# Performance work log

Measured on AMD Instinct MI355X. Metric: run time of the kernel, lower is better.

The kernel has to match this reference:

```python
import jax, jax.numpy as jnp
import numpy as np

B, N, U = 4096, 128, 128  # batch, num_notes, num_units
F = N - 1                 # per-note feature dim; +1 condition scalar -> LSTM input = N
W_SCALE = 0.08            # ~1/sqrt(U), keeps gates in a sane range


def setup_inputs() -> dict:
    key = jax.random.key(0)
    ks = jax.random.split(key, 12)
    return {
        "note_features": jax.random.normal(ks[0], (B, N, F), jnp.float32),
        "targets": jax.random.uniform(ks[1], (B, N), jnp.float32),
        "w_ih0": jax.random.normal(ks[2], (4 * U, N), jnp.float32) * W_SCALE,
        "w_hh0": jax.random.normal(ks[3], (4 * U, U), jnp.float32) * W_SCALE,
        "b_ih0": jax.random.normal(ks[4], (4 * U,), jnp.float32) * W_SCALE,
        "b_hh0": jax.random.normal(ks[5], (4 * U,), jnp.float32) * W_SCALE,
        "w_ih1": jax.random.normal(ks[6], (4 * U, U), jnp.float32) * W_SCALE,
        "w_hh1": jax.random.normal(ks[7], (4 * U, U), jnp.float32) * W_SCALE,
        "b_ih1": jax.random.normal(ks[8], (4 * U,), jnp.float32) * W_SCALE,
        "b_hh1": jax.random.normal(ks[9], (4 * U,), jnp.float32) * W_SCALE,
        "w_out": jax.random.normal(ks[10], (1, U), jnp.float32) * W_SCALE,
        "b_out": jax.random.normal(ks[11], (1,), jnp.float32) * W_SCALE,
    }


def _lstm_cell(x, h, c, w_ih, w_hh, b_ih, b_hh):
    # PyTorch gate order: i, f, g, o
    gates = x @ w_ih.T + b_ih + h @ w_hh.T + b_hh  # [B, 4U]
    i, f, g, o = jnp.split(gates, 4, axis=-1)
    c_new = jax.nn.sigmoid(f) * c + jax.nn.sigmoid(i) * jnp.tanh(g)
    h_new = jax.nn.sigmoid(o) * jnp.tanh(c_new)
    return h_new, c_new


def reference(note_features, targets, w_ih0, w_hh0, b_ih0, b_hh0,
              w_ih1, w_hh1, b_ih1, b_hh1, w_out, b_out):
    b = note_features.shape[0]
    # teacher-forced condition: previous target note, zero at step 0
    cond = jnp.concatenate([jnp.zeros((b, 1), note_features.dtype), targets[:, :-1]], axis=1)
    x_seq = jnp.concatenate([note_features, cond[..., None]], axis=-1)  # [B, N, N]
    x_seq = jnp.transpose(x_seq, (1, 0, 2))                              # [N, B, N]

    zeros = jnp.zeros((b, U), note_features.dtype)

    def step(carry, x):
        h0, c0, h1, c1 = carry
        h0, c0 = _lstm_cell(x, h0, c0, w_ih0, w_hh0, b_ih0, b_hh0)
        h1, c1 = _lstm_cell(h0, h1, c1, w_ih1, w_hh1, b_ih1, b_hh1)
        return (h0, c0, h1, c1), h1

    _, hs = jax.lax.scan(step, (zeros, zeros, zeros, zeros), x_seq)  # [N, B, U]
    logits = jnp.einsum('nbu,ou->nbo', hs, w_out) + b_out            # [N, B, 1]
    return jnp.transpose(jax.nn.sigmoid(logits)[..., 0], (1, 0))     # [B, N]
```

## Files before the change

### kernel.cpp

```cpp
#include <hip/hip_runtime.h>
#include <math.h>

typedef _Float16 f16;
typedef _Float16 f16x8 __attribute__((ext_vector_type(8)));
typedef float f32x4 __attribute__((ext_vector_type(4)));

#define NSTEP 128
#define FEAT  127
#define BLK_B 16
#define NBLOCK 256
#define NTHREADS 512

__device__ __forceinline__ float sigf(float x) { return 1.0f / (1.0f + __expf(-x)); }
__device__ __forceinline__ float tanh_(float x) { return 1.0f - 2.0f / (1.0f + __expf(2.0f * x)); }

__device__ __forceinline__ void sync_lds() {
    asm volatile("s_waitcnt lgkmcnt(0)" ::: "memory");
    __builtin_amdgcn_s_barrier();
    asm volatile("" ::: "memory");
}

#define PIN(v) asm volatile("" : "+v"(v))

__device__ __forceinline__ f16x8 load_wfrag(const float* __restrict__ W, int n, int k) {
    const float* p = W + n * 128 + k;
    f16x8 r;
#pragma unroll
    for (int j = 0; j < 8; ++j) r[j] = (f16)p[j];
    return r;
}

__device__ __forceinline__ float row16_sum(float v) {
    int t;
    t = __builtin_amdgcn_update_dpp(0, __float_as_int(v), 0x118, 0xf, 0xf, true);
    v += __int_as_float(t);
    t = __builtin_amdgcn_update_dpp(0, __float_as_int(v), 0x114, 0xf, 0xf, true);
    v += __int_as_float(t);
    t = __builtin_amdgcn_update_dpp(0, __float_as_int(v), 0x112, 0xf, 0xf, true);
    v += __int_as_float(t);
    t = __builtin_amdgcn_update_dpp(0, __float_as_int(v), 0x111, 0xf, 0xf, true);
    v += __int_as_float(t);
    return v;
}

__global__ __launch_bounds__(NTHREADS, 2) void lstm_fused(
    const float* __restrict__ nf,    const float* __restrict__ tgt,
    const float* __restrict__ w_ih0, const float* __restrict__ w_hh0,
    const float* __restrict__ b_ih0, const float* __restrict__ b_hh0,
    const float* __restrict__ w_ih1, const float* __restrict__ w_hh1,
    const float* __restrict__ b_ih1, const float* __restrict__ b_hh1,
    const float* __restrict__ w_out, const float* __restrict__ b_out,
    f16* __restrict__ h0g, float* __restrict__ out)
{
    __shared__ __align__(16) f16 bufA[2][16][152];
    __shared__ __align__(16) f16 bufB[2][16][152];
    __shared__ float outp[2][8][16];

    const int tid  = threadIdx.x;
    const int wave = tid >> 6;
    const int lane = tid & 63;
    const int col  = lane & 15;
    const int quad = lane >> 4;
    const int b0   = blockIdx.x * BLK_B;
    const int u    = wave * 16 + col;
    const f32x4 zz = {0.f, 0.f, 0.f, 0.f};

    {
        for (int i = tid; i < 2 * 16 * 152; i += NTHREADS)
            (&bufB[0][0][0])[i] = (f16)0.0f;

        f32x4 bv0[4];
#pragma unroll
        for (int g = 0; g < 4; ++g) {
            const float b = b_ih0[g * 128 + u] + b_hh0[g * 128 + u];
            bv0[g] = (f32x4){b, b, b, b};
        }

        f16x8 wih0[4][4], whh0[4][4];
#pragma unroll
        for (int g = 0; g < 4; ++g)
#pragma unroll
            for (int ks = 0; ks < 4; ++ks) {
                wih0[g][ks] = load_wfrag(w_ih0, g * 128 + u, ks * 32 + quad * 8);
                whh0[g][ks] = load_wfrag(w_hh0, g * 128 + u, ks * 32 + quad * 8);
                PIN(wih0[g][ks]);
                PIN(whh0[g][ks]);
            }

        const float* px[2][2];
        int pxs[2][2];
#pragma unroll
        for (int rr = 0; rr < 2; ++rr) {
            const long rowg = b0 + wave * 2 + rr;
#pragma unroll
            for (int h = 0; h < 2; ++h) {
                const int k = lane + 64 * h;
                if (k < FEAT) { px[rr][h] = nf + (rowg * NSTEP + 2) * FEAT + k; pxs[rr][h] = FEAT; }
                else          { px[rr][h] = tgt + rowg * NSTEP + 1;             pxs[rr][h] = 1; }
            }
        }

        f16* hp = h0g + (long)(b0 + quad * 4) * NSTEP * 128 + u;

        f32x4 c0 = {0.f, 0.f, 0.f, 0.f};

#pragma unroll
        for (int rr = 0; rr < 2; ++rr) {
            const int row = wave * 2 + rr;
            const long gbt = (long)(b0 + row) * NSTEP;
#pragma unroll
            for (int h = 0; h < 2; ++h) {
                const int k = lane + 64 * h;
                bufA[0][row][k] = (f16)((k < FEAT) ? nf[gbt * FEAT + k] : 0.0f);
            }
        }

        float xb0[2][2], xb1[2][2];
#pragma unroll
        for (int rr = 0; rr < 2; ++rr) {
            const long rowg = b0 + wave * 2 + rr;
#pragma unroll
            for (int h = 0; h < 2; ++h) {
                const int k = lane + 64 * h;
                xb1[rr][h] = (k < FEAT) ? nf[(rowg * NSTEP + 1) * FEAT + k]
                                        : tgt[rowg * NSTEP];
            }
        }
        sync_lds();

        auto step0 = [&](int t, int pa, float (&xIssue)[2][2], float (&xWrite)[2][2]) {
            const int wb = pa ^ 1;

            if (t + 2 < NSTEP) {
#pragma unroll
                for (int rr = 0; rr < 2; ++rr)
#pragma unroll
                    for (int h = 0; h < 2; ++h) {
                        xIssue[rr][h] = *px[rr][h];
                        px[rr][h] += pxs[rr][h];
                    }
            }

            f16x8 ax[4], ah[4];
#pragma unroll
            for (int ks = 0; ks < 4; ++ks) {
                ax[ks] = *(const f16x8*)&bufA[pa][col][ks * 32 + quad * 8];
                ah[ks] = *(const f16x8*)&bufB[pa][col][ks * 32 + quad * 8];
            }

            f32x4 accx[4], acch[4];
#pragma unroll
            for (int g = 0; g < 4; ++g) {
                accx[g] = __builtin_amdgcn_mfma_f32_16x16x32_f16(ax[0], wih0[g][0], bv0[g], 0, 0, 0);
                acch[g] = __builtin_amdgcn_mfma_f32_16x16x32_f16(ah[0], whh0[g][0], zz, 0, 0, 0);
            }
#pragma unroll
            for (int ks = 1; ks < 4; ++ks)
#pragma unroll
                for (int g = 0; g < 4; ++g) {
                    accx[g] = __builtin_amdgcn_mfma_f32_16x16x32_f16(ax[ks], wih0[g][ks], accx[g], 0, 0, 0);
                    acch[g] = __builtin_amdgcn_mfma_f32_16x16x32_f16(ah[ks], whh0[g][ks], acch[g], 0, 0, 0);
                }

            float h0n[4];
#pragma unroll
            for (int r = 0; r < 4; ++r) {
                const float ig = sigf(accx[0][r] + acch[0][r]);
                const float fg = sigf(accx[1][r] + acch[1][r]);
                const float gg = tanh_(accx[2][r] + acch[2][r]);
                const float og = sigf(accx[3][r] + acch[3][r]);
                const float cn = fg * c0[r] + ig * gg;
                c0[r] = cn;
                h0n[r] = og * tanh_(cn);
            }
#pragma unroll
            for (int r = 0; r < 4; ++r) {
                bufB[wb][quad * 4 + r][u] = (f16)h0n[r];
                hp[r * (NSTEP * 128)] = (f16)h0n[r];
            }
            hp += 128;

            if (t + 1 < NSTEP) {
#pragma unroll
                for (int rr = 0; rr < 2; ++rr)
#pragma unroll
                    for (int h = 0; h < 2; ++h)
                        bufA[wb][wave * 2 + rr][lane + 64 * h] = (f16)xWrite[rr][h];
            }
            sync_lds();
        };

        for (int t2 = 0; t2 < NSTEP; t2 += 2) {
            step0(t2,     0, xb0, xb1);
            step0(t2 + 1, 1, xb1, xb0);
        }
    }

    __syncthreads();
    for (int i = tid; i < 2 * 16 * 152; i += NTHREADS)
        (&bufA[0][0][0])[i] = (f16)0.0f;
    __syncthreads();

    {
        f32x4 bv1[4];
#pragma unroll
        for (int g = 0; g < 4; ++g) {
            const float b = b_ih1[g * 128 + u] + b_hh1[g * 128 + u];
            bv1[g] = (f32x4){b, b, b, b};
        }
        const float wo_u = w_out[u];
        const float bout = b_out[0];

        f16x8 wih1[4][4], whh1[4][4];
#pragma unroll
        for (int g = 0; g < 4; ++g)
#pragma unroll
            for (int ks = 0; ks < 4; ++ks) {
                wih1[g][ks] = load_wfrag(w_ih1, g * 128 + u, ks * 32 + quad * 8);
                whh1[g][ks] = load_wfrag(w_hh1, g * 128 + u, ks * 32 + quad * 8);
                PIN(wih1[g][ks]);
                PIN(whh1[g][ks]);
            }

        f32x4 c1 = {0.f, 0.f, 0.f, 0.f};

        const f16* hrow = h0g + (long)(b0 + col) * NSTEP * 128 + quad * 8;
        f16x8 nxA[4], nxB[4];
#pragma unroll
        for (int ks = 0; ks < 4; ++ks)
            nxA[ks] = *(const f16x8*)(hrow + ks * 32);
#pragma unroll
        for (int ks = 0; ks < 4; ++ks)
            nxB[ks] = *(const f16x8*)(hrow + 128 + ks * 32);
        const f16* hnext = hrow + 256;

        auto step1 = [&](int t, int pa, f16x8 (&nxUse)[4]) {
            const int wb = pa ^ 1;

            f16x8 ahv[4];
#pragma unroll
            for (int ks = 0; ks < 4; ++ks)
                ahv[ks] = *(const f16x8*)&bufA[pa][col][ks * 32 + quad * 8];

            f32x4 accx[4], acch[4];
#pragma unroll
            for (int g = 0; g < 4; ++g) {
                accx[g] = __builtin_amdgcn_mfma_f32_16x16x32_f16(nxUse[0], wih1[g][0], bv1[g], 0, 0, 0);
                acch[g] = __builtin_amdgcn_mfma_f32_16x16x32_f16(ahv[0], whh1[g][0], zz, 0, 0, 0);
            }
#pragma unroll
            for (int ks = 1; ks < 4; ++ks)
#pragma unroll
                for (int g = 0; g < 4; ++g) {
                    accx[g] = __builtin_amdgcn_mfma_f32_16x16x32_f16(nxUse[ks], wih1[g][ks], accx[g], 0, 0, 0);
                    acch[g] = __builtin_amdgcn_mfma_f32_16x16x32_f16(ahv[ks], whh1[g][ks], acch[g], 0, 0, 0);
                }

            if (t + 2 < NSTEP) {
#pragma unroll
                for (int ks = 0; ks < 4; ++ks)
                    nxUse[ks] = *(const f16x8*)(hnext + ks * 32);
                hnext += 128;
            }

            float h1n[4];
#pragma unroll
            for (int r = 0; r < 4; ++r) {
                const float ig = sigf(accx[0][r] + acch[0][r]);
                const float fg = sigf(accx[1][r] + acch[1][r]);
                const float gg = tanh_(accx[2][r] + acch[2][r]);
                const float og = sigf(accx[3][r] + acch[3][r]);
                const float cn = fg * c1[r] + ig * gg;
                c1[r] = cn;
                h1n[r] = og * tanh_(cn);
            }
#pragma unroll
            for (int r = 0; r < 4; ++r)
                bufA[wb][quad * 4 + r][u] = (f16)h1n[r];

            float ps[4];
#pragma unroll
            for (int r = 0; r < 4; ++r) ps[r] = row16_sum(h1n[r] * wo_u);
            if (col == 15) {
#pragma unroll
                for (int r = 0; r < 4; ++r) outp[pa][wave][quad * 4 + r] = ps[r];
            }

            sync_lds();

            if (tid < 16) {
                float s = bout;
#pragma unroll
                for (int w = 0; w < 8; ++w) s += outp[pa][w][tid];
                out[(long)(b0 + tid) * NSTEP + t] = sigf(s);
            }
        };

        for (int t2 = 0; t2 < NSTEP; t2 += 2) {
            step1(t2,     0, nxA);
            step1(t2 + 1, 1, nxB);
        }
    }
}

__global__ void prep_weights(const float* __restrict__ w_ih0,
                             const float* __restrict__ w_hh0,
                             const float* __restrict__ w_ih1,
                             const float* __restrict__ w_hh1,
                             f16* __restrict__ ws16)
{
    int idx = blockIdx.x * blockDim.x + threadIdx.x;
    int j    = idx & 7;
    int lane = (idx >> 3) & 63;
    int ks   = (idx >> 9) & 3;
    int gate = (idx >> 11) & 3;
    int wave = (idx >> 13) & 7;
    int sel  = (idx >> 16) & 3;
    int n = gate * 128 + wave * 16 + (lane & 15);
    int k = ks * 32 + (lane >> 4) * 8 + j;
    const float* W = (sel == 0) ? w_ih0 : (sel == 1) ? w_hh0 : (sel == 2) ? w_ih1 : w_hh1;
    ws16[idx] = (f16)W[n * 128 + k];
}

__global__ __launch_bounds__(NTHREADS, 2) void lstm_fb(
    const float* __restrict__ nf,   const float* __restrict__ tgt,
    const float* __restrict__ b_ih0, const float* __restrict__ b_hh0,
    const float* __restrict__ b_ih1, const float* __restrict__ b_hh1,
    const float* __restrict__ w_out, const float* __restrict__ b_out,
    const f16* __restrict__ wfrag,  float* __restrict__ out)
{
    __shared__ f16 xs[2][16][152];
    __shared__ f16 h0s[2][16][152];
    __shared__ f16 h1s[2][16][152];
    __shared__ float outp[8][16];

    const int tid  = threadIdx.x;
    const int wave = tid >> 6;
    const int lane = tid & 63;
    const int col  = lane & 15;
    const int quad = lane >> 4;
    const int b0   = blockIdx.x * BLK_B;
    const int u    = wave * 16 + col;

    for (int i = tid; i < 2 * 16 * 152; i += NTHREADS) {
        (&h0s[0][0][0])[i] = (f16)0.0f;
        (&h1s[0][0][0])[i] = (f16)0.0f;
    }
    float bias0[4], bias1[4];
#pragma unroll
    for (int g = 0; g < 4; ++g) {
        bias0[g] = b_ih0[g * 128 + u] + b_hh0[g * 128 + u];
        bias1[g] = b_ih1[g * 128 + u] + b_hh1[g * 128 + u];
    }
    const float wo_u = w_out[u];
    const float bout = b_out[0];
    const f16x8* wf = (const f16x8*)wfrag;

    f32x4 c0 = {0.f, 0.f, 0.f, 0.f};
    f32x4 c1 = {0.f, 0.f, 0.f, 0.f};

#pragma unroll
    for (int rr = 0; rr < 2; ++rr) {
        const int row = wave * 2 + rr;
        const long gbt = (long)(b0 + row) * NSTEP;
#pragma unroll
        for (int h = 0; h < 2; ++h) {
            const int k = lane + 64 * h;
            xs[0][row][k] = (f16)((k < FEAT) ? nf[gbt * FEAT + k] : 0.0f);
        }
    }
    __syncthreads();

    for (int t = 0; t < NSTEP; ++t) {
        const int pa = t & 1, wb = pa ^ 1;
        float xnv[2][2];
#pragma unroll
        for (int rr = 0; rr < 2; ++rr) {
            const int row = wave * 2 + rr;
#pragma unroll
            for (int h = 0; h < 2; ++h) {
                const int k = lane + 64 * h;
                float v = 0.0f;
                if (t + 1 < NSTEP) {
                    const long gbt = (long)(b0 + row) * NSTEP + (t + 1);
                    v = (k < FEAT) ? nf[gbt * FEAT + k] : tgt[(long)(b0 + row) * NSTEP + t];
                }
                xnv[rr][h] = v;
            }
        }
        f32x4 acc[4];
#pragma unroll
        for (int g = 0; g < 4; ++g) acc[g] = (f32x4){bias0[g], bias0[g], bias0[g], bias0[g]};
#pragma unroll
        for (int ks = 0; ks < 4; ++ks) {
            f16x8 a = *(const f16x8*)&xs[pa][col][ks * 32 + quad * 8];
#pragma unroll
            for (int g = 0; g < 4; ++g) {
                f16x8 b = wf[((wave * 4 + g) * 4 + ks) * 64 + lane];
                acc[g] = __builtin_amdgcn_mfma_f32_16x16x32_f16(a, b, acc[g], 0, 0, 0);
            }
        }
#pragma unroll
        for (int ks = 0; ks < 4; ++ks) {
            f16x8 a = *(const f16x8*)&h0s[pa][col][ks * 32 + quad * 8];
#pragma unroll
            for (int g = 0; g < 4; ++g) {
                f16x8 b = wf[1 * 8192 + ((wave * 4 + g) * 4 + ks) * 64 + lane];
                acc[g] = __builtin_amdgcn_mfma_f32_16x16x32_f16(a, b, acc[g], 0, 0, 0);
            }
        }
        float h0n[4];
#pragma unroll
        for (int r = 0; r < 4; ++r) {
            const float ig = sigf(acc[0][r]);
            const float fg = sigf(acc[1][r]);
            const float gg = tanh_(acc[2][r]);
            const float og = sigf(acc[3][r]);
            const float cn = fg * c0[r] + ig * gg;
            c0[r] = cn;
            h0n[r] = og * tanh_(cn);
        }
#pragma unroll
        for (int r = 0; r < 4; ++r) h0s[wb][quad * 4 + r][u] = (f16)h0n[r];
        __syncthreads();

#pragma unroll
        for (int g = 0; g < 4; ++g) acc[g] = (f32x4){bias1[g], bias1[g], bias1[g], bias1[g]};
#pragma unroll
        for (int ks = 0; ks < 4; ++ks) {
            f16x8 a = *(const f16x8*)&h0s[wb][col][ks * 32 + quad * 8];
#pragma unroll
            for (int g = 0; g < 4; ++g) {
                f16x8 b = wf[2 * 8192 + ((wave * 4 + g) * 4 + ks) * 64 + lane];
                acc[g] = __builtin_amdgcn_mfma_f32_16x16x32_f16(a, b, acc[g], 0, 0, 0);
            }
        }
#pragma unroll
        for (int ks = 0; ks < 4; ++ks) {
            f16x8 a = *(const f16x8*)&h1s[pa][col][ks * 32 + quad * 8];
#pragma unroll
            for (int g = 0; g < 4; ++g) {
                f16x8 b = wf[3 * 8192 + ((wave * 4 + g) * 4 + ks) * 64 + lane];
                acc[g] = __builtin_amdgcn_mfma_f32_16x16x32_f16(a, b, acc[g], 0, 0, 0);
            }
        }
        float h1n[4];
#pragma unroll
        for (int r = 0; r < 4; ++r) {
            const float ig = sigf(acc[0][r]);
            const float fg = sigf(acc[1][r]);
            const float gg = tanh_(acc[2][r]);
            const float og = sigf(acc[3][r]);
            const float cn = fg * c1[r] + ig * gg;
            c1[r] = cn;
            h1n[r] = og * tanh_(cn);
        }
#pragma unroll
        for (int r = 0; r < 4; ++r) h1s[wb][quad * 4 + r][u] = (f16)h1n[r];
#pragma unroll
        for (int rr = 0; rr < 2; ++rr) {
            const int row = wave * 2 + rr;
#pragma unroll
            for (int h = 0; h < 2; ++h) xs[wb][row][lane + 64 * h] = (f16)xnv[rr][h];
        }
        float ps[4];
#pragma unroll
        for (int r = 0; r < 4; ++r) ps[r] = h1n[r] * wo_u;
#pragma unroll
        for (int m = 1; m < 16; m <<= 1) {
#pragma unroll
            for (int r = 0; r < 4; ++r) ps[r] += __shfl_xor(ps[r], m, 64);
        }
        if (col == 0) {
#pragma unroll
            for (int r = 0; r < 4; ++r) outp[wave][quad * 4 + r] = ps[r];
        }
        __syncthreads();
        if (tid < 16) {
            float s = bout;
#pragma unroll
            for (int w = 0; w < 8; ++w) s += outp[w][tid];
            out[(long)(b0 + tid) * NSTEP + t] = sigf(s);
        }
    }
}

extern "C" void kernel_launch(void* const* d_in, const int* in_sizes, int n_in,
                              void* d_out, int out_size, void* d_ws, size_t ws_size,
                              hipStream_t stream)
{
    const float* nf    = (const float*)d_in[0];
    const float* tgt   = (const float*)d_in[1];
    const float* w_ih0 = (const float*)d_in[2];
    const float* w_hh0 = (const float*)d_in[3];
    const float* b_ih0 = (const float*)d_in[4];
    const float* b_hh0 = (const float*)d_in[5];
    const float* w_ih1 = (const float*)d_in[6];
    const float* w_hh1 = (const float*)d_in[7];
    const float* b_ih1 = (const float*)d_in[8];
    const float* b_hh1 = (const float*)d_in[9];
    const float* w_out = (const float*)d_in[10];
    const float* b_out = (const float*)d_in[11];

    float* out = (float*)d_out;

    const size_t need = (size_t)4096 * 128 * 128 * 2;
    if (ws_size >= need) {
        f16* h0g = (f16*)d_ws;
        lstm_fused<<<NBLOCK, NTHREADS, 0, stream>>>(
            nf, tgt, w_ih0, w_hh0, b_ih0, b_hh0,
            w_ih1, w_hh1, b_ih1, b_hh1, w_out, b_out, h0g, out);
    } else {
        f16* ws16 = (f16*)d_ws;
        prep_weights<<<1024, 256, 0, stream>>>(w_ih0, w_hh0, w_ih1, w_hh1, ws16);
        lstm_fb<<<NBLOCK, NTHREADS, 0, stream>>>(nf, tgt, b_ih0, b_hh0, b_ih1, b_hh1,
                                                 w_out, b_out, ws16, out);
    }
}
```

Measured before the change: 781.0 us.

## Merge both LSTM layers into one wavefront-skewed kernel with LDS-resident weights

Adds a merged kernel that runs layer 0 at step t and layer 1 at step t-1 in the same iteration. This replaces the two-phase approach that wrote every h0 to global memory and then read it back. Three weight matrices stay in registers and w_ih1 is staged in 128KB of dynamic LDS, removing the global h0 round trip and halving the sequential barrier chain. The risk is higher register and LDS pressure: 128KB of LDS per block likely limits occupancy to one block per CU, and every iteration now adds LDS weight reads. The old fallback kernel is removed.

```diff
diff --git a/kernel.cpp b/kernel.cpp
--- a/kernel.cpp
+++ b/kernel.cpp
@@ -43,6 +43,243 @@
     return v;
 }
 
+#define LWIDX(wv, g, ks, ln) (((((wv) * 4 + (g)) * 4 + (ks)) * 64) + (ln))
+
+__global__ __launch_bounds__(NTHREADS, 2) void lstm_merged(
+    const float* __restrict__ nf,    const float* __restrict__ tgt,
+    const float* __restrict__ w_ih0, const float* __restrict__ w_hh0,
+    const float* __restrict__ b_ih0, const float* __restrict__ b_hh0,
+    const float* __restrict__ w_ih1, const float* __restrict__ w_hh1,
+    const float* __restrict__ b_ih1, const float* __restrict__ b_hh1,
+    const float* __restrict__ w_out, const float* __restrict__ b_out,
+    float* __restrict__ out)
+{
+    extern __shared__ __align__(16) f16 dynlds[];
+    __shared__ __align__(16) f16 bufX[2][16][152];
+    __shared__ __align__(16) f16 bufH0[2][16][152];
+    __shared__ __align__(16) f16 bufH1[2][16][152];
+    __shared__ float outp[2][8][16];
+
+    const int tid  = threadIdx.x;
+    const int wave = tid >> 6;
+    const int lane = tid & 63;
+    const int col  = lane & 15;
+    const int quad = lane >> 4;
+    const int b0   = blockIdx.x * BLK_B;
+    const int u    = wave * 16 + col;
+    const f32x4 zz = {0.f, 0.f, 0.f, 0.f};
+
+    f16x8* lwp = (f16x8*)dynlds;
+    const f16x8* lw = (const f16x8*)dynlds;
+
+    for (int i = tid; i < 2 * 16 * 152; i += NTHREADS) {
+        (&bufH0[0][0][0])[i] = (f16)0.0f;
+        (&bufH1[0][0][0])[i] = (f16)0.0f;
+    }
+
+    float bias0[4], bias1[4];
+#pragma unroll
+    for (int g = 0; g < 4; ++g) {
+        bias0[g] = b_ih0[g * 128 + u] + b_hh0[g * 128 + u];
+        bias1[g] = b_ih1[g * 128 + u] + b_hh1[g * 128 + u];
+    }
+    const float wo_u = w_out[u];
+    const float bout = b_out[0];
+
+    f16x8 wih0[4][4], whh0[4][4], whh1[4][4];
+#pragma unroll
+    for (int g = 0; g < 4; ++g)
+#pragma unroll
+        for (int ks = 0; ks < 4; ++ks) {
+            wih0[g][ks] = load_wfrag(w_ih0, g * 128 + u, ks * 32 + quad * 8);
+            whh0[g][ks] = load_wfrag(w_hh0, g * 128 + u, ks * 32 + quad * 8);
+            whh1[g][ks] = load_wfrag(w_hh1, g * 128 + u, ks * 32 + quad * 8);
+            PIN(wih0[g][ks]);
+            PIN(whh0[g][ks]);
+            PIN(whh1[g][ks]);
+        }
+
+#pragma unroll
+    for (int g = 0; g < 4; ++g)
+#pragma unroll
+        for (int ks = 0; ks < 4; ++ks)
+            lwp[LWIDX(wave, g, ks, lane)] = load_wfrag(w_ih1, g * 128 + u, ks * 32 + quad * 8);
+
+    const float* px[2][2];
+    int pxs[2][2];
+#pragma unroll
+    for (int rr = 0; rr < 2; ++rr) {
+        const long rowg = b0 + wave * 2 + rr;
+#pragma unroll
+        for (int h = 0; h < 2; ++h) {
+            const int k = lane + 64 * h;
+            if (k < FEAT) { px[rr][h] = nf + (rowg * NSTEP + 2) * FEAT + k; pxs[rr][h] = FEAT; }
+            else          { px[rr][h] = tgt + rowg * NSTEP + 1;             pxs[rr][h] = 1; }
+        }
+    }
+
+    f32x4 c0 = {0.f, 0.f, 0.f, 0.f};
+    f32x4 c1 = {0.f, 0.f, 0.f, 0.f};
+
+    float xb0[2][2], xb1[2][2];
+#pragma unroll
+    for (int rr = 0; rr < 2; ++rr) {
+        const int row = wave * 2 + rr;
+        const long gbt = (long)(b0 + row) * NSTEP;
+#pragma unroll
+        for (int h = 0; h < 2; ++h) {
+            const int k = lane + 64 * h;
+            bufX[0][row][k] = (f16)((k < FEAT) ? nf[gbt * FEAT + k] : 0.0f);
+            xb1[rr][h] = (k < FEAT) ? nf[(gbt + 1) * FEAT + k] : tgt[gbt];
+        }
+    }
+    sync_lds();
+
+    auto iter = [&](int t, int pa, float (&xIssue)[2][2], float (&xWrite)[2][2]) {
+        const int wb = pa ^ 1;
+        const bool hasL0 = (t < NSTEP);
+        const bool hasL1 = (t >= 1);
+
+        f16x8 ah[4];
+#pragma unroll
+        for (int ks = 0; ks < 4; ++ks)
+            ah[ks] = *(const f16x8*)&bufH0[pa][col][ks * 32 + quad * 8];
+
+        if (hasL0) {
+            if (t + 2 < NSTEP) {
+#pragma unroll
+                for (int rr = 0; rr < 2; ++rr)
+#pragma unroll
+                    for (int h = 0; h < 2; ++h) {
+                        xIssue[rr][h] = *px[rr][h];
+                        px[rr][h] += pxs[rr][h];
+                    }
+            }
+
+            f16x8 ax[4];
+#pragma unroll
+            for (int ks = 0; ks < 4; ++ks)
+                ax[ks] = *(const f16x8*)&bufX[pa][col][ks * 32 + quad * 8];
+
+            f32x4 accx[4], acch[4];
+#pragma unroll
+            for (int g = 0; g < 4; ++g) {
+                f32x4 bv = {bias0[g], bias0[g], bias0[g], bias0[g]};
+                accx[g] = __builtin_amdgcn_mfma_f32_16x16x32_f16(ax[0], wih0[g][0], bv, 0, 0, 0);
+                acch[g] = __builtin_amdgcn_mfma_f32_16x16x32_f16(ah[0], whh0[g][0], zz, 0, 0, 0);
+            }
+#pragma unroll
+            for (int ks = 1; ks < 4; ++ks)
+#pragma unroll
+                for (int g = 0; g < 4; ++g) {
+                    accx[g] = __builtin_amdgcn_mfma_f32_16x16x32_f16(ax[ks], wih0[g][ks], accx[g], 0, 0, 0);
+                    acch[g] = __builtin_amdgcn_mfma_f32_16x16x32_f16(ah[ks], whh0[g][ks], acch[g], 0, 0, 0);
+                }
+
+            float h0n[4];
+#pragma unroll
+            for (int r = 0; r < 4; ++r) {
+                const float ig = sigf(accx[0][r] + acch[0][r]);
+                const float fg = sigf(accx[1][r] + acch[1][r]);
+                const float gg = tanh_(accx[2][r] + acch[2][r]);
+                const float og = sigf(accx[3][r] + acch[3][r]);
+                const float cn = fg * c0[r] + ig * gg;
+                c0[r] = cn;
+                h0n[r] = og * tanh_(cn);
+            }
+#pragma unroll
+            for (int r = 0; r < 4; ++r)
+                bufH0[wb][quad * 4 + r][u] = (f16)h0n[r];
+        }
+
+        if (hasL1) {
+            f16x8 ah1[4];
+#pragma unroll
+            for (int ks = 0; ks < 4; ++ks)
+                ah1[ks] = *(const f16x8*)&bufH1[pa][col][ks * 32 + quad * 8];
+
+            f32x4 accx[4], acch[4];
+            {
+                f16x8 w0 = lw[LWIDX(wave, 0, 0, lane)];
+                f16x8 w1 = lw[LWIDX(wave, 1, 0, lane)];
+                f16x8 w2 = lw[LWIDX(wave, 2, 0, lane)];
+                f16x8 w3 = lw[LWIDX(wave, 3, 0, lane)];
+                f32x4 bv0_ = {bias1[0], bias1[0], bias1[0], bias1[0]};
+                f32x4 bv1_ = {bias1[1], bias1[1], bias1[1], bias1[1]};
+                f32x4 bv2_ = {bias1[2], bias1[2], bias1[2], bias1[2]};
+                f32x4 bv3_ = {bias1[3], bias1[3], bias1[3], bias1[3]};
+                accx[0] = __builtin_amdgcn_mfma_f32_16x16x32_f16(ah[0], w0, bv0_, 0, 0, 0);
+                accx[1] = __builtin_amdgcn_mfma_f32_16x16x32_f16(ah[0], w1, bv1_, 0, 0, 0);
+                accx[2] = __builtin_amdgcn_mfma_f32_16x16x32_f16(ah[0], w2, bv2_, 0, 0, 0);
+                accx[3] = __builtin_amdgcn_mfma_f32_16x16x32_f16(ah[0], w3, bv3_, 0, 0, 0);
+            }
+#pragma unroll
+            for (int g = 0; g < 4; ++g)
+                acch[g] = __builtin_amdgcn_mfma_f32_16x16x32_f16(ah1[0], whh1[g][0], zz, 0, 0, 0);
+#pragma unroll
+            for (int ks = 1; ks < 4; ++ks) {
+                f16x8 w0 = lw[LWIDX(wave, 0, ks, lane)];
+                f16x8 w1 = lw[LWIDX(wave, 1, ks, lane)];
+                f16x8 w2 = lw[LWIDX(wave, 2, ks, lane)];
+                f16x8 w3 = lw[LWIDX(wave, 3, ks, lane)];
+                accx[0] = __builtin_amdgcn_mfma_f32_16x16x32_f16(ah[ks], w0, accx[0], 0, 0, 0);
+                accx[1] = __builtin_amdgcn_mfma_f32_16x16x32_f16(ah[ks], w1, accx[1], 0, 0, 0);
+                accx[2] = __builtin_amdgcn_mfma_f32_16x16x32_f16(ah[ks], w2, accx[2], 0, 0, 0);
+                accx[3] = __builtin_amdgcn_mfma_f32_16x16x32_f16(ah[ks], w3, accx[3], 0, 0, 0);
+#pragma unroll
+                for (int g = 0; g < 4; ++g)
+                    acch[g] = __builtin_amdgcn_mfma_f32_16x16x32_f16(ah1[ks], whh1[g][ks], acch[g], 0, 0, 0);
+            }
+
+            float h1n[4];
+#pragma unroll
+            for (int r = 0; r < 4; ++r) {
+                const float ig = sigf(accx[0][r] + acch[0][r]);
+                const float fg = sigf(accx[1][r] + acch[1][r]);
+                const float gg = tanh_(accx[2][r] + acch[2][r]);
+                const float og = sigf(accx[3][r] + acch[3][r]);
+                const float cn = fg * c1[r] + ig * gg;
+                c1[r] = cn;
+                h1n[r] = og * tanh_(cn);
+            }
+#pragma unroll
+            for (int r = 0; r < 4; ++r)
+                bufH1[wb][quad * 4 + r][u] = (f16)h1n[r];
+
+            float ps[4];
+#pragma unroll
+            for (int r = 0; r < 4; ++r) ps[r] = row16_sum(h1n[r] * wo_u);
+            if (col == 15) {
+#pragma unroll
+                for (int r = 0; r < 4; ++r) outp[pa][wave][quad * 4 + r] = ps[r];
+            }
+        }
+
+        if (t + 1 < NSTEP) {
+#pragma unroll
+            for (int rr = 0; rr < 2; ++rr)
+#pragma unroll
+                for (int h = 0; h < 2; ++h)
+                    bufX[wb][wave * 2 + rr][lane + 64 * h] = (f16)xWrite[rr][h];
+        }
+
+        sync_lds();
+
+        if (hasL1 && tid < 16) {
+            float s = bout;
+#pragma unroll
+            for (int w = 0; w < 8; ++w) s += outp[pa][w][tid];
+            out[(long)(b0 + tid) * NSTEP + (t - 1)] = sigf(s);
+        }
+    };
+
+    for (int t2 = 0; t2 <= NSTEP; t2 += 2) {
+        iter(t2, 0, xb0, xb1);
+        if (t2 + 1 <= NSTEP)
+            iter(t2 + 1, 1, xb1, xb0);
+    }
+}
+
 __global__ __launch_bounds__(NTHREADS, 2) void lstm_fused(
     const float* __restrict__ nf,    const float* __restrict__ tgt,
     const float* __restrict__ w_ih0, const float* __restrict__ w_hh0,
@@ -101,7 +338,6 @@
         }
 
         f16* hp = h0g + (long)(b0 + quad * 4) * NSTEP * 128 + u;
-
         f32x4 c0 = {0.f, 0.f, 0.f, 0.f};
 
 #pragma unroll
@@ -130,7 +366,6 @@
 
         auto step0 = [&](int t, int pa, float (&xIssue)[2][2], float (&xWrite)[2][2]) {
             const int wb = pa ^ 1;
-
             if (t + 2 < NSTEP) {
 #pragma unroll
                 for (int rr = 0; rr < 2; ++rr)
@@ -140,14 +375,12 @@
                         px[rr][h] += pxs[rr][h];
                     }
             }
-
             f16x8 ax[4], ah[4];
 #pragma unroll
             for (int ks = 0; ks < 4; ++ks) {
                 ax[ks] = *(const f16x8*)&bufA[pa][col][ks * 32 + quad * 8];
                 ah[ks] = *(const f16x8*)&bufB[pa][col][ks * 32 + quad * 8];
             }
-
             f32x4 accx[4], acch[4];
 #pragma unroll
             for (int g = 0; g < 4; ++g) {
@@ -161,7 +394,6 @@
                     accx[g] = __builtin_amdgcn_mfma_f32_16x16x32_f16(ax[ks], wih0[g][ks], accx[g], 0, 0, 0);
                     acch[g] = __builtin_amdgcn_mfma_f32_16x16x32_f16(ah[ks], whh0[g][ks], acch[g], 0, 0, 0);
                 }
-
             float h0n[4];
 #pragma unroll
             for (int r = 0; r < 4; ++r) {
@@ -179,7 +411,6 @@
                 hp[r * (NSTEP * 128)] = (f16)h0n[r];
             }
             hp += 128;
-
             if (t + 1 < NSTEP) {
 #pragma unroll
                 for (int rr = 0; rr < 2; ++rr)
@@ -223,7 +454,6 @@
             }
 
         f32x4 c1 = {0.f, 0.f, 0.f, 0.f};
-
         const f16* hrow = h0g + (long)(b0 + col) * NSTEP * 128 + quad * 8;
         f16x8 nxA[4], nxB[4];
 #pragma unroll
@@ -236,12 +466,10 @@
 
         auto step1 = [&](int t, int pa, f16x8 (&nxUse)[4]) {
             const int wb = pa ^ 1;
-
             f16x8 ahv[4];
 #pragma unroll
             for (int ks = 0; ks < 4; ++ks)
                 ahv[ks] = *(const f16x8*)&bufA[pa][col][ks * 32 + quad * 8];
-
             f32x4 accx[4], acch[4];
 #pragma unroll
             for (int g = 0; g < 4; ++g) {
@@ -255,14 +483,12 @@
                     accx[g] = __builtin_amdgcn_mfma_f32_16x16x32_f16(nxUse[ks], wih1[g][ks], accx[g], 0, 0, 0);
                     acch[g] = __builtin_amdgcn_mfma_f32_16x16x32_f16(ahv[ks], whh1[g][ks], acch[g], 0, 0, 0);
                 }
-
             if (t + 2 < NSTEP) {
 #pragma unroll
                 for (int ks = 0; ks < 4; ++ks)
                     nxUse[ks] = *(const f16x8*)(hnext + ks * 32);
                 hnext += 128;
             }
-
             float h1n[4];
 #pragma unroll
             for (int r = 0; r < 4; ++r) {
@@ -277,7 +503,6 @@
 #pragma unroll
             for (int r = 0; r < 4; ++r)
                 bufA[wb][quad * 4 + r][u] = (f16)h1n[r];
-
             float ps[4];
 #pragma unroll
             for (int r = 0; r < 4; ++r) ps[r] = row16_sum(h1n[r] * wo_u);
@@ -285,9 +510,7 @@
 #pragma unroll
                 for (int r = 0; r < 4; ++r) outp[pa][wave][quad * 4 + r] = ps[r];
             }
-
             sync_lds();
-
             if (tid < 16) {
                 float s = bout;
 #pragma unroll
@@ -299,188 +522,6 @@
         for (int t2 = 0; t2 < NSTEP; t2 += 2) {
             step1(t2,     0, nxA);
             step1(t2 + 1, 1, nxB);
-        }
-    }
-}
-
-__global__ void prep_weights(const float* __restrict__ w_ih0,
-                             const float* __restrict__ w_hh0,
-                             const float* __restrict__ w_ih1,
-                             const float* __restrict__ w_hh1,
-                             f16* __restrict__ ws16)
-{
-    int idx = blockIdx.x * blockDim.x + threadIdx.x;
-    int j    = idx & 7;
-    int lane = (idx >> 3) & 63;
-    int ks   = (idx >> 9) & 3;
-    int gate = (idx >> 11) & 3;
-    int wave = (idx >> 13) & 7;
-    int sel  = (idx >> 16) & 3;
-    int n = gate * 128 + wave * 16 + (lane & 15);
-    int k = ks * 32 + (lane >> 4) * 8 + j;
-    const float* W = (sel == 0) ? w_ih0 : (sel == 1) ? w_hh0 : (sel == 2) ? w_ih1 : w_hh1;
-    ws16[idx] = (f16)W[n * 128 + k];
-}
-
-__global__ __launch_bounds__(NTHREADS, 2) void lstm_fb(
-    const float* __restrict__ nf,   const float* __restrict__ tgt,
-    const float* __restrict__ b_ih0, const float* __restrict__ b_hh0,
-    const float* __restrict__ b_ih1, const float* __restrict__ b_hh1,
-    const float* __restrict__ w_out, const float* __restrict__ b_out,
-    const f16* __restrict__ wfrag,  float* __restrict__ out)
-{
-    __shared__ f16 xs[2][16][152];
-    __shared__ f16 h0s[2][16][152];
-    __shared__ f16 h1s[2][16][152];
-    __shared__ float outp[8][16];
-
-    const int tid  = threadIdx.x;
-    const int wave = tid >> 6;
-    const int lane = tid & 63;
-    const int col  = lane & 15;
-    const int quad = lane >> 4;
-    const int b0   = blockIdx.x * BLK_B;
-    const int u    = wave * 16 + col;
-
-    for (int i = tid; i < 2 * 16 * 152; i += NTHREADS) {
-        (&h0s[0][0][0])[i] = (f16)0.0f;
-        (&h1s[0][0][0])[i] = (f16)0.0f;
-    }
-    float bias0[4], bias1[4];
-#pragma unroll
-    for (int g = 0; g < 4; ++g) {
-        bias0[g] = b_ih0[g * 128 + u] + b_hh0[g * 128 + u];
-        bias1[g] = b_ih1[g * 128 + u] + b_hh1[g * 128 + u];
-    }
-    const float wo_u = w_out[u];
-    const float bout = b_out[0];
-    const f16x8* wf = (const f16x8*)wfrag;
-
-    f32x4 c0 = {0.f, 0.f, 0.f, 0.f};
-    f32x4 c1 = {0.f, 0.f, 0.f, 0.f};
-
-#pragma unroll
-    for (int rr = 0; rr < 2; ++rr) {
-        const int row = wave * 2 + rr;
-        const long gbt = (long)(b0 + row) * NSTEP;
-#pragma unroll
-        for (int h = 0; h < 2; ++h) {
-            const int k = lane + 64 * h;
-            xs[0][row][k] = (f16)((k < FEAT) ? nf[gbt * FEAT + k] : 0.0f);
-        }
-    }
-    __syncthreads();
-
-    for (int t = 0; t < NSTEP; ++t) {
-        const int pa = t & 1, wb = pa ^ 1;
-        float xnv[2][2];
-#pragma unroll
-        for (int rr = 0; rr < 2; ++rr) {
-            const int row = wave * 2 + rr;
-#pragma unroll
-            for (int h = 0; h < 2; ++h) {
-                const int k = lane + 64 * h;
-                float v = 0.0f;
-                if (t + 1 < NSTEP) {
-                    const long gbt = (long)(b0 + row) * NSTEP + (t + 1);
-                    v = (k < FEAT) ? nf[gbt * FEAT + k] : tgt[(long)(b0 + row) * NSTEP + t];
-                }
-                xnv[rr][h] = v;
-            }
-        }
-        f32x4 acc[4];
-#pragma unroll
-        for (int g = 0; g < 4; ++g) acc[g] = (f32x4){bias0[g], bias0[g], bias0[g], bias0[g]};
-#pragma unroll
-        for (int ks = 0; ks < 4; ++ks) {
-            f16x8 a = *(const f16x8*)&xs[pa][col][ks * 32 + quad * 8];
-#pragma unroll
-            for (int g = 0; g < 4; ++g) {
-                f16x8 b = wf[((wave * 4 + g) * 4 + ks) * 64 + lane];
-                acc[g] = __builtin_amdgcn_mfma_f32_16x16x32_f16(a, b, acc[g], 0, 0, 0);
-            }
-        }
-#pragma unroll
-        for (int ks = 0; ks < 4; ++ks) {
-            f16x8 a = *(const f16x8*)&h0s[pa][col][ks * 32 + quad * 8];
-#pragma unroll
-            for (int g = 0; g < 4; ++g) {
-                f16x8 b = wf[1 * 8192 + ((wave * 4 + g) * 4 + ks) * 64 + lane];
-                acc[g] = __builtin_amdgcn_mfma_f32_16x16x32_f16(a, b, acc[g], 0, 0, 0);
-            }
-        }
-        float h0n[4];
-#pragma unroll
-        for (int r = 0; r < 4; ++r) {
-            const float ig = sigf(acc[0][r]);
-            const float fg = sigf(acc[1][r]);
-            const float gg = tanh_(acc[2][r]);
-            const float og = sigf(acc[3][r]);
-            const float cn = fg * c0[r] + ig * gg;
-            c0[r] = cn;
-            h0n[r] = og * tanh_(cn);
-        }
-#pragma unroll
-        for (int r = 0; r < 4; ++r) h0s[wb][quad * 4 + r][u] = (f16)h0n[r];
-        __syncthreads();
-
-#pragma unroll
-        for (int g = 0; g < 4; ++g) acc[g] = (f32x4){bias1[g], bias1[g], bias1[g], bias1[g]};
-#pragma unroll
-        for (int ks = 0; ks < 4; ++ks) {
-            f16x8 a = *(const f16x8*)&h0s[wb][col][ks * 32 + quad * 8];
-#pragma unroll
-            for (int g = 0; g < 4; ++g) {
-                f16x8 b = wf[2 * 8192 + ((wave * 4 + g) * 4 + ks) * 64 + lane];
-                acc[g] = __builtin_amdgcn_mfma_f32_16x16x32_f16(a, b, acc[g], 0, 0, 0);
-            }
-        }
-#pragma unroll
-        for (int ks = 0; ks < 4; ++ks) {
-            f16x8 a = *(const f16x8*)&h1s[pa][col][ks * 32 + quad * 8];
-#pragma unroll
-            for (int g = 0; g < 4; ++g) {
-                f16x8 b = wf[3 * 8192 + ((wave * 4 + g) * 4 + ks) * 64 + lane];
-                acc[g] = __builtin_amdgcn_mfma_f32_16x16x32_f16(a, b, acc[g], 0, 0, 0);
-            }
-        }
-        float h1n[4];
-#pragma unroll
-        for (int r = 0; r < 4; ++r) {
-            const float ig = sigf(acc[0][r]);
-            const float fg = sigf(acc[1][r]);
-            const float gg = tanh_(acc[2][r]);
-            const float og = sigf(acc[3][r]);
-            const float cn = fg * c1[r] + ig * gg;
-            c1[r] = cn;
-            h1n[r] = og * tanh_(cn);
-        }
-#pragma unroll
-        for (int r = 0; r < 4; ++r) h1s[wb][quad * 4 + r][u] = (f16)h1n[r];
-#pragma unroll
-        for (int rr = 0; rr < 2; ++rr) {
-            const int row = wave * 2 + rr;
-#pragma unroll
-            for (int h = 0; h < 2; ++h) xs[wb][row][lane + 64 * h] = (f16)xnv[rr][h];
-        }
-        float ps[4];
-#pragma unroll
-        for (int r = 0; r < 4; ++r) ps[r] = h1n[r] * wo_u;
-#pragma unroll
-        for (int m = 1; m < 16; m <<= 1) {
-#pragma unroll
-            for (int r = 0; r < 4; ++r) ps[r] += __shfl_xor(ps[r], m, 64);
-        }
-        if (col == 0) {
-#pragma unroll
-            for (int r = 0; r < 4; ++r) outp[wave][quad * 4 + r] = ps[r];
-        }
-        __syncthreads();
-        if (tid < 16) {
-            float s = bout;
-#pragma unroll
-            for (int w = 0; w < 8; ++w) s += outp[w][tid];
-            out[(long)(b0 + tid) * NSTEP + t] = sigf(s);
         }
     }
 }
@@ -504,16 +545,23 @@
 
     float* out = (float*)d_out;
 
+    static int merged_ok = -1;
+    if (merged_ok < 0) {
+        hipError_t e = hipFuncSetAttribute(
+            reinterpret_cast<const void*>(lstm_merged),
+            hipFuncAttributeMaxDynamicSharedMemorySize, 131072);
+        merged_ok = (e == hipSuccess) ? 1 : 0;
+    }
+
     const size_t need = (size_t)4096 * 128 * 128 * 2;
-    if (ws_size >= need) {
+    if (merged_ok) {
+        lstm_merged<<<NBLOCK, NTHREADS, 131072, stream>>>(
+            nf, tgt, w_ih0, w_hh0, b_ih0, b_hh0,
+            w_ih1, w_hh1, b_ih1, b_hh1, w_out, b_out, out);
+    } else if (ws_size >= need) {
         f16* h0g = (f16*)d_ws;
         lstm_fused<<<NBLOCK, NTHREADS, 0, stream>>>(
             nf, tgt, w_ih0, w_hh0, b_ih0, b_hh0,
             w_ih1, w_hh1, b_ih1, b_hh1, w_out, b_out, h0g, out);
-    } else {
-        f16* ws16 = (f16*)d_ws;
-        prep_weights<<<1024, 256, 0, stream>>>(w_ih0, w_hh0, w_ih1, w_hh1, ws16);
-        lstm_fb<<<NBLOCK, NTHREADS, 0, stream>>>(nf, tgt, b_ih0, b_hh0, b_ih1, b_hh1,
-                                                 w_out, b_out, ws16, out);
     }
 }
```

After: 1.717 ms. +119.9%, slower.
